# Optimization experiments

Hardware: AMD Instinct MI355X
Metric: run time of the kernel (lower is better)

The kernel has to match this reference:

```python
import jax, jax.numpy as jnp
import numpy as np

B, C, H, W = 128, 32, 64, 64
L = H * W  # 4096
RATE = L * C  # 131072


def setup_inputs() -> dict:
    key = jax.random.key(0)
    k1, k2, k3, k4 = jax.random.split(key, 4)
    x = jax.random.normal(k1, (B, C, H, W), dtype=jnp.float32)
    px = jax.random.normal(k2, (1,), dtype=jnp.float32)
    # kaiming_normal_(a=sqrt(5)) on a (RATE, C) matrix: fan_in = C,
    # gain = sqrt(2/(1+a^2)) = sqrt(2/6), std = gain/sqrt(fan_in)
    std = np.sqrt(2.0 / 6.0) / np.sqrt(C)
    weight = jax.random.normal(k3, (RATE, C), dtype=jnp.float32) * std
    bound = 1.0 / np.sqrt(C)
    bias = jax.random.uniform(k4, (RATE,), dtype=jnp.float32, minval=-bound, maxval=bound)
    return {"x": x, "px": px, "weight": weight, "bias": bias}


def reference(x, px, weight, bias):
    b_, c_, h_, w_ = x.shape
    l_ = h_ * w_
    # [B, C, H, W] -> [B, L, C]
    x_blc = x.reshape(b_, c_, l_).transpose(0, 2, 1)
    w = weight.reshape(l_, c_, c_)   # per-position [C, C] weight
    b = bias.reshape(l_, c_)         # per-position bias
    # per-position batched matmul: (B,L,1,C) @ (L,C,C) -> (B,L,C)
    out = jnp.einsum('blc,lcd->bld', x_blc, w) + b
    # [B, L, C] -> [B, C, H, W]
    return out.reshape(b_, h_, w_, c_).transpose(0, 3, 1, 2)
```

## Files before the change

kernel.cpp:

```cpp
#include <hip/hip_runtime.h>
#include <stdint.h>


namespace {

constexpr int kC  = 32;
constexpr int kL  = 4096;
constexpr int kNB = 4;
constexpr int kND = 8;
constexpr int kCC = 2;
constexpr int kLB = 64;
constexpr int kChunks = kC / kCC;
constexpr int kChunkFloats = kLB * kCC * kC;

__device__ __forceinline__ void async_ld16(const float* g, float* l) {
    __builtin_amdgcn_global_load_lds(
        (__attribute__((address_space(1))) const void*)g,
        (__attribute__((address_space(3))) void*)l, 16, 0, 0);
}

__global__ __launch_bounds__(256, 4)
void dyna_dec(const float* __restrict__ x,
              const float* __restrict__ w,
              const float* __restrict__ bias,
              float* __restrict__ out) {
    __shared__ __align__(16) float ldsA[kChunkFloats];
    __shared__ __align__(16) float ldsB[kChunkFloats];

    const int tid = threadIdx.x;
    const int lt  = tid & 63;
    const int dg  = tid >> 6;
    const int l   = blockIdx.x * kLB + lt;
    const int b0  = blockIdx.y * kNB;
    const int d0  = dg * kND;

    const float* xp = x + (size_t)b0 * (kC * kL) + l;
    const float* wb = w + (size_t)blockIdx.x * kLB * (kC * kC);

    int goff[4];
    const int ldsbase = dg * 1024;
#pragma unroll
    for (int k = 0; k < 4; ++k) {
        const int s   = dg * 256 + k * 64 + lt;
        const int ls  = s >> 4;
        const int cs  = (s >> 3) & 1;
        const int dsl = s & 7;
        goff[k] = ls * (kC * kC) + cs * kC + ((dsl ^ (ls & 7)) << 2);
    }

    auto stage = [&](float* buf, int cb) {
#pragma unroll
        for (int k = 0; k < 4; ++k)
            async_ld16(wb + cb * (kCC * kC) + goff[k], buf + ldsbase + k * 256);
    };

    float xrA[kCC][kNB], xrB[kCC][kNB];
    auto xload = [&](float (&xr)[kCC][kNB], int cb) {
#pragma unroll
        for (int c = 0; c < kCC; ++c)
#pragma unroll
            for (int i = 0; i < kNB; ++i)
                xr[c][i] = xp[(size_t)i * (kC * kL) +
                              (size_t)(cb * kCC + c) * kL];
    };

    float acc[kNB][kND];
#pragma unroll
    for (int i = 0; i < kNB; ++i)
#pragma unroll
        for (int j = 0; j < kND; ++j) acc[i][j] = 0.0f;

    auto compute = [&](const float* buf, const float (&xr)[kCC][kNB]) {
#pragma unroll
        for (int c = 0; c < kCC; ++c) {
            const int sl0 = lt * 16 + c * 8 + ((2 * dg) ^ (lt & 7));
            const int sl1 = lt * 16 + c * 8 + ((2 * dg + 1) ^ (lt & 7));
            const float4 w0 = *reinterpret_cast<const float4*>(buf + sl0 * 4);
            const float4 w1 = *reinterpret_cast<const float4*>(buf + sl1 * 4);
#pragma unroll
            for (int i = 0; i < kNB; ++i) {
                const float xv = xr[c][i];
                acc[i][0] += xv * w0.x;
                acc[i][1] += xv * w0.y;
                acc[i][2] += xv * w0.z;
                acc[i][3] += xv * w0.w;
                acc[i][4] += xv * w1.x;
                acc[i][5] += xv * w1.y;
                acc[i][6] += xv * w1.z;
                acc[i][7] += xv * w1.w;
            }
        }
    };

    stage(ldsA, 0);
    xload(xrA, 0);
    __syncthreads();

#pragma unroll 1
    for (int t = 0; t < kChunks / 2; ++t) {
        const int cbE = 2 * t;
        stage(ldsB, cbE + 1);
        xload(xrB, cbE + 1);
        compute(ldsA, xrA);
        __syncthreads();
        if (t < kChunks / 2 - 1) {
            stage(ldsA, cbE + 2);
            xload(xrA, cbE + 2);
        }
        compute(ldsB, xrB);
        __syncthreads();
    }

    const float4 b0v = *reinterpret_cast<const float4*>(bias + (size_t)l * kC + d0);
    const float4 b1v = *reinterpret_cast<const float4*>(bias + (size_t)l * kC + d0 + 4);
    const float bv[kND] = {b0v.x, b0v.y, b0v.z, b0v.w, b1v.x, b1v.y, b1v.z, b1v.w};

#pragma unroll
    for (int i = 0; i < kNB; ++i) {
        float* op = out + (size_t)(b0 + i) * (kC * kL) + l;
#pragma unroll
        for (int j = 0; j < kND; ++j)
            op[(size_t)(d0 + j) * kL] = acc[i][j] + bv[j];
    }
}

}

extern "C" void kernel_launch(void* const* d_in, const int* in_sizes, int n_in,
                              void* d_out, int out_size, void* d_ws, size_t ws_size,
                              hipStream_t stream) {
    const float* x    = (const float*)d_in[0];
    const float* wgt  = (const float*)d_in[2];
    const float* bias = (const float*)d_in[3];
    float* out = (float*)d_out;

    dim3 grid(kL / 64, 128 / kNB);
    dim3 block(256);
    hipLaunchKernelGGL(dyna_dec, grid, block, 0, stream, x, wgt, bias, out);
}
```

Baseline: 166.1 us.

## Deepen x prefetch and use explicit vmcnt waits for LDS staging pipeline

Restructures the double-buffered loop into a manually unrolled schedule that prefetches x values two chunks ahead and replaces __syncthreads with s_waitcnt vmcnt plus raw s_barrier and scheduling fences. Partial vmcnt waits let the weight LDS stage complete while x global loads stay in flight, so compute can overlap those loads. It adds register pressure from the doubled x buffers, and correctness depends on the hand-counted wait values.

```diff
diff --git a/kernel.cpp b/kernel.cpp
--- a/kernel.cpp
+++ b/kernel.cpp
@@ -10,7 +10,6 @@
 constexpr int kND = 8;
 constexpr int kCC = 2;
 constexpr int kLB = 64;
-constexpr int kChunks = kC / kCC;
 constexpr int kChunkFloats = kLB * kCC * kC;
 
 __device__ __forceinline__ void async_ld16(const float* g, float* l) {
@@ -18,6 +17,11 @@
         (__attribute__((address_space(1))) const void*)g,
         (__attribute__((address_space(3))) void*)l, 16, 0, 0);
 }
+
+#define WAITV0()  asm volatile("s_waitcnt vmcnt(0)" ::: "memory")
+#define WAITV16() asm volatile("s_waitcnt vmcnt(16)" ::: "memory")
+#define SCHEDFENCE() __builtin_amdgcn_sched_barrier(0)
+#define BARRIER() do { __builtin_amdgcn_s_barrier(); SCHEDFENCE(); } while (0)
 
 __global__ __launch_bounds__(256, 4)
 void dyna_dec(const float* __restrict__ x,
@@ -54,14 +58,16 @@
             async_ld16(wb + cb * (kCC * kC) + goff[k], buf + ldsbase + k * 256);
     };
 
-    float xrA[kCC][kNB], xrB[kCC][kNB];
-    auto xload = [&](float (&xr)[kCC][kNB], int cb) {
+    float xr0[2][kCC][kNB], xr1[2][kCC][kNB];
+    auto xload2 = [&](float (&xr)[2][kCC][kNB], int chunk0) {
 #pragma unroll
-        for (int c = 0; c < kCC; ++c)
+        for (int h = 0; h < 2; ++h)
 #pragma unroll
-            for (int i = 0; i < kNB; ++i)
-                xr[c][i] = xp[(size_t)i * (kC * kL) +
-                              (size_t)(cb * kCC + c) * kL];
+            for (int c = 0; c < kCC; ++c)
+#pragma unroll
+                for (int i = 0; i < kNB; ++i)
+                    xr[h][c][i] = xp[(size_t)i * (kC * kL) +
+                                     (size_t)((chunk0 + h) * kCC + c) * kL];
     };
 
     float acc[kNB][kND];
@@ -93,23 +99,36 @@
     };
 
     stage(ldsA, 0);
-    xload(xrA, 0);
-    __syncthreads();
+    SCHEDFENCE();
+    xload2(xr0, 0);
 
 #pragma unroll 1
-    for (int t = 0; t < kChunks / 2; ++t) {
-        const int cbE = 2 * t;
-        stage(ldsB, cbE + 1);
-        xload(xrB, cbE + 1);
-        compute(ldsA, xrA);
-        __syncthreads();
-        if (t < kChunks / 2 - 1) {
-            stage(ldsA, cbE + 2);
-            xload(xrA, cbE + 2);
-        }
-        compute(ldsB, xrB);
-        __syncthreads();
+    for (int q = 0; q < 3; ++q) {
+        const int t0 = 4 * q;
+        WAITV0(); BARRIER();
+        stage(ldsB, t0 + 1); SCHEDFENCE(); xload2(xr1, t0 + 2);
+        compute(ldsA, xr0[0]);
+        WAITV16(); BARRIER();
+        stage(ldsA, t0 + 2);
+        compute(ldsB, xr0[1]);
+        WAITV0(); BARRIER();
+        stage(ldsB, t0 + 3); SCHEDFENCE(); xload2(xr0, t0 + 4);
+        compute(ldsA, xr1[0]);
+        WAITV16(); BARRIER();
+        stage(ldsA, t0 + 4);
+        compute(ldsB, xr1[1]);
     }
+    WAITV0(); BARRIER();
+    stage(ldsB, 13); SCHEDFENCE(); xload2(xr1, 14);
+    compute(ldsA, xr0[0]);
+    WAITV16(); BARRIER();
+    stage(ldsA, 14);
+    compute(ldsB, xr0[1]);
+    WAITV0(); BARRIER();
+    stage(ldsB, 15);
+    compute(ldsA, xr1[0]);
+    WAITV0(); BARRIER();
+    compute(ldsB, xr1[1]);
 
     const float4 b0v = *reinterpret_cast<const float4*>(bias + (size_t)l * kC + d0);
     const float4 b1v = *reinterpret_cast<const float4*>(bias + (size_t)l * kC + d0 + 4);
```

After: 276.2 us. +66.2%, slower.
